# Performance work log

Hardware: AMD Instinct MI355X
Metric: run time of the kernel (lower is better)

Reference implementation:

```python
import jax, jax.numpy as jnp
import numpy as np


def setup_inputs() -> dict:
    key = jax.random.key(0)
    k1, k2, k3, k4 = jax.random.split(key, 4)
    B, n_env, in_ch, out_ch, code_ch, modes1, L = 16, 8, 32, 32, 16, 64, 8192
    scale = 1.0 / (in_ch * out_ch)
    return {
        "x": jax.random.normal(k1, (B, n_env * in_ch, L), dtype=jnp.float32),
        "codes": jax.random.normal(k2, (n_env, code_ch), dtype=jnp.float32),
        "com_weights": scale * jax.random.uniform(k3, (in_ch, out_ch, modes1, 2), dtype=jnp.float32),
        "code_weights": scale * jax.random.uniform(k4, (code_ch * in_ch, out_ch, modes1, 2), dtype=jnp.float32),
        "filter_weights": -3.0 * jnp.ones((modes1,), dtype=jnp.float32),
    }


def _as_complex(w):
    return w[..., 0] + 1j * w[..., 1]


def reference(x, codes, com_weights, code_weights, filter_weights):
    B, C, L = x.shape
    n_env, code_ch = codes.shape
    in_ch = C // n_env
    out_ch = com_weights.shape[1]
    modes1 = com_weights.shape[2]
    n_freq = L // 2 + 1

    # FFT and reshape to [B, e, i, freq]
    x_ft = jnp.fft.rfft(x).reshape(B, n_env, in_ch, n_freq)
    xm = x_ft[..., :modes1]  # mode truncation

    cw = _as_complex(com_weights)  # [i, o, m]
    codew = _as_complex(code_weights.reshape(code_ch, in_ch, out_ch, modes1, 2))  # [c,i,o,m]
    env_w = jnp.einsum('ec,ciom->eiom', codes.astype(codew.dtype), codew)

    # hardsigmoid(filter_weights): clip(x/6 + 0.5, 0, 1)
    lam = jnp.clip(filter_weights / 6.0 + 0.5, 0.0, 1.0)  # [m]

    out_m = (lam * jnp.einsum('beim,iom->beom', xm, cw)
             + (1.0 - lam) * jnp.einsum('beim,eiom->beom', xm, env_w))  # [B,e,o,m]

    # zero-pad back to full spectrum then inverse FFT
    out_ft = jnp.zeros((B, n_env, out_ch, n_freq), dtype=out_m.dtype)
    out_ft = out_ft.at[..., :modes1].set(out_m)
    out_ft = out_ft.reshape(B, n_env * out_ch, n_freq)
    return jnp.fft.irfft(out_ft, n=L)
```

## Files before the change

### kernel.cpp

```cpp
#include <hip/hip_runtime.h>
#include <hip/hip_bf16.h>
#include <math.h>
#include <stdint.h>

typedef __bf16 bf16_t;
typedef __bf16 bf16x8 __attribute__((ext_vector_type(8)));
typedef float  f32x4  __attribute__((ext_vector_type(4)));

#define L_LEN 8192
#define MODES 64
#define NCOMP 128
#define M_ROWS 4096

__device__ __forceinline__ void g2lds16(const void* g, void* l) {
  __builtin_amdgcn_global_load_lds(
      (__attribute__((address_space(1))) void*)(uintptr_t)(g),
      (__attribute__((address_space(3))) void*)(l), 16, 0, 0);
}

__global__ void gen_basis(bf16_t* __restrict__ B1t, bf16_t* __restrict__ B1) {
  int id = blockIdx.x * 256 + threadIdx.x;
  int l = id >> 6;
  int k = id & 63;
  int r = (l * k) & (L_LEN - 1);
  float ang = (float)r * 7.6699039394282061e-4f;
  float s, c;
  sincosf(ang, &s, &c);
  B1 [l * NCOMP + k]             = (bf16_t)c;
  B1 [l * NCOMP + MODES + k]     = (bf16_t)(-s);
  B1t[(size_t)k * L_LEN + l]           = (bf16_t)c;
  B1t[(size_t)(MODES + k) * L_LEN + l] = (bf16_t)(-s);
}

__global__ void wmix(const float* __restrict__ codes, const float* __restrict__ comw,
                     const float* __restrict__ codew, const float* __restrict__ fw,
                     float* __restrict__ W) {
  int id = blockIdx.x * 256 + threadIdx.x;
  int k = id & 63;
  int o = (id >> 6) & 31;
  int i = (id >> 11) & 31;
  int e = id >> 16;
  float lam = fminf(fmaxf(fw[k] * (1.0f / 6.0f) + 0.5f, 0.0f), 1.0f);
  float are = 0.f, aim = 0.f;
#pragma unroll
  for (int c = 0; c < 16; ++c) {
    float cd = codes[e * 16 + c];
    const float* p = codew + ((((c * 32 + i) * 32 + o) * 64 + k) << 1);
    are += cd * p[0];
    aim += cd * p[1];
  }
  const float* q = comw + (((i * 32 + o) * 64 + k) << 1);
  float wre = lam * q[0] + (1.f - lam) * are;
  float wim = lam * q[1] + (1.f - lam) * aim;
  float* dst = W + ((((e * 32 + i) * 32 + o) * 64 + k) << 1);
  dst[0] = wre;
  dst[1] = wim;
}

__global__ __launch_bounds__(256) void stage1(const float* __restrict__ x,
                                              const bf16_t* __restrict__ B1t,
                                              float* __restrict__ X) {
  __shared__ bf16_t Al[128 * 72];
  __shared__ bf16_t Bl[128 * 64];
  const int t = threadIdx.x;
  const int lane = t & 63;
  const int w = t >> 6;
  const int wm = w >> 1, wn = w & 1;
  const int mt = blockIdx.x;
  const int sp = blockIdx.y;
  const int lq = lane >> 4;
  const int l15 = lane & 15;

  f32x4 acc[4][4];
#pragma unroll
  for (int a = 0; a < 4; ++a)
#pragma unroll
    for (int b = 0; b < 4; ++b) acc[a][b] = (f32x4){0.f, 0.f, 0.f, 0.f};

  const int r = t >> 1, half = t & 1;
  const float* xrow = x + (size_t)(mt * 128 + r) * L_LEN + half * 32;
  bf16_t* adst = Al + r * 72 + half * 32;

  for (int ch = 0; ch < 8; ++ch) {
    const int l0 = sp * 512 + ch * 64;
    __syncthreads();
    const float4* xp = (const float4*)(xrow + l0);
#pragma unroll
    for (int j = 0; j < 4; ++j) {
      float4 p0 = xp[2 * j], p1 = xp[2 * j + 1];
      bf16x8 v = {(bf16_t)p0.x, (bf16_t)p0.y, (bf16_t)p0.z, (bf16_t)p0.w,
                  (bf16_t)p1.x, (bf16_t)p1.y, (bf16_t)p1.z, (bf16_t)p1.w};
      *(bf16x8*)(adst + j * 8) = v;
    }
#pragma unroll
    for (int q2 = 0; q2 < 4; ++q2) {
      int slot = t + 256 * q2;
      int n  = slot >> 3;
      int m8 = slot & 7;
      int j8 = m8 ^ (n & 7);
      g2lds16(B1t + (size_t)n * L_LEN + l0 + j8 * 8, (char*)Bl + slot * 16);
    }
    __syncthreads();
#pragma unroll
    for (int s = 0; s < 2; ++s) {
      bf16x8 a[4], b[4];
#pragma unroll
      for (int mf = 0; mf < 4; ++mf) {
        int row = wm * 64 + mf * 16 + l15;
        a[mf] = *(const bf16x8*)(Al + row * 72 + s * 32 + lq * 8);
      }
#pragma unroll
      for (int nf = 0; nf < 4; ++nf) {
        int n = wn * 64 + nf * 16 + l15;
        int j8 = (s * 4 + lq) ^ (n & 7);
        b[nf] = *(const bf16x8*)(Bl + n * 64 + j8 * 8);
      }
#pragma unroll
      for (int mf = 0; mf < 4; ++mf)
#pragma unroll
        for (int nf = 0; nf < 4; ++nf)
          acc[mf][nf] = __builtin_amdgcn_mfma_f32_16x16x32_bf16(a[mf], b[nf], acc[mf][nf], 0, 0, 0);
    }
  }
#pragma unroll
  for (int mf = 0; mf < 4; ++mf)
#pragma unroll
    for (int nf = 0; nf < 4; ++nf) {
      int n = wn * 64 + nf * 16 + l15;
#pragma unroll
      for (int rg = 0; rg < 4; ++rg) {
        int m = mt * 128 + wm * 64 + mf * 16 + lq * 4 + rg;
        atomicAdd(X + (size_t)m * NCOMP + n, acc[mf][nf][rg]);
      }
    }
}

__global__ __launch_bounds__(256) void mixk(const float* __restrict__ X,
                                            const float* __restrict__ W,
                                            bf16_t* __restrict__ A2) {
  __shared__ float Xs[32 * 128];
  const int t = threadIdx.x;
  const int be = blockIdx.x;
  const int e = be & 7;
#pragma unroll
  for (int j = 0; j < 16; ++j) {
    int idx = t + 256 * j;
    Xs[idx] = X[(size_t)be * 4096 + idx];
  }
  __syncthreads();
  const int k = t & 63;
  const int olo = t >> 6;
  float yre[8], yim[8];
#pragma unroll
  for (int j = 0; j < 8; ++j) { yre[j] = 0.f; yim[j] = 0.f; }
  for (int i = 0; i < 32; ++i) {
    float xr = Xs[i * 128 + k];
    float xi = Xs[i * 128 + 64 + k];
    const float* wp = W + ((((e * 32 + i) * 32 + olo * 8) * 64 + k) << 1);
#pragma unroll
    for (int j = 0; j < 8; ++j) {
      float2 wv = *(const float2*)(wp + j * 128);
      yre[j] += xr * wv.x - xi * wv.y;
      yim[j] += xr * wv.y + xi * wv.x;
    }
  }
  float sc = (k == 0) ? (1.0f / 8192.0f) : (2.0f / 8192.0f);
#pragma unroll
  for (int j = 0; j < 8; ++j) {
    int m = be * 32 + olo * 8 + j;
    A2[m * NCOMP + k]         = (bf16_t)(yre[j] * sc);
    A2[m * NCOMP + MODES + k] = (bf16_t)(yim[j] * sc);
  }
}

__global__ __launch_bounds__(256) void stage2(const bf16_t* __restrict__ A2,
                                              const bf16_t* __restrict__ B1,
                                              float* __restrict__ out) {
  __shared__ bf16_t As[128 * 128];
  __shared__ bf16_t Bs[128 * 128];
  const int t = threadIdx.x;
  const int lane = t & 63;
  const int w = t >> 6;
  const int wm = w >> 1, wl = w & 1;
  const int lt = blockIdx.x, mt = blockIdx.y;
  const int lq = lane >> 4, l15 = lane & 15;

#pragma unroll
  for (int q2 = 0; q2 < 8; ++q2) {
    int slot = t + 256 * q2;
    int row = slot >> 4;
    int m16 = slot & 15;
    int j8 = m16 ^ (row & 15);
    g2lds16(A2 + (size_t)(mt * 128 + row) * NCOMP + j8 * 8, (char*)As + slot * 16);
  }
#pragma unroll
  for (int q2 = 0; q2 < 8; ++q2) {
    int slot = t + 256 * q2;
    int lr = slot >> 4;
    int m16 = slot & 15;
    int j8 = m16 ^ (lr & 15);
    g2lds16(B1 + (size_t)(lt * 128 + lr) * NCOMP + j8 * 8, (char*)Bs + slot * 16);
  }
  __syncthreads();

  f32x4 acc[4][4];
#pragma unroll
  for (int a = 0; a < 4; ++a)
#pragma unroll
    for (int b = 0; b < 4; ++b) acc[a][b] = (f32x4){0.f, 0.f, 0.f, 0.f};

#pragma unroll
  for (int s = 0; s < 4; ++s) {
    bf16x8 a[4], b[4];
#pragma unroll
    for (int mf = 0; mf < 4; ++mf) {
      int row = wm * 64 + mf * 16 + l15;
      a[mf] = *(const bf16x8*)(As + row * 128 + (((s * 4 + lq) ^ (row & 15)) * 8));
    }
#pragma unroll
    for (int nf = 0; nf < 4; ++nf) {
      int lr = wl * 64 + nf * 16 + l15;
      b[nf] = *(const bf16x8*)(Bs + lr * 128 + (((s * 4 + lq) ^ (lr & 15)) * 8));
    }
#pragma unroll
    for (int mf = 0; mf < 4; ++mf)
#pragma unroll
      for (int nf = 0; nf < 4; ++nf)
        acc[mf][nf] = __builtin_amdgcn_mfma_f32_16x16x32_bf16(a[mf], b[nf], acc[mf][nf], 0, 0, 0);
  }

#pragma unroll
  for (int mf = 0; mf < 4; ++mf)
#pragma unroll
    for (int nf = 0; nf < 4; ++nf) {
      int m = mt * 128 + wm * 64 + mf * 16 + lq * 4;
      int l = lt * 128 + wl * 64 + nf * 16 + l15;
      float* op = out + (size_t)m * L_LEN + l;
#pragma unroll
      for (int rg = 0; rg < 4; ++rg) op[(size_t)rg * L_LEN] = acc[mf][nf][rg];
    }
}

extern "C" void kernel_launch(void* const* d_in, const int* in_sizes, int n_in,
                              void* d_out, int out_size, void* d_ws, size_t ws_size,
                              hipStream_t stream) {
  const float* x     = (const float*)d_in[0];
  const float* codes = (const float*)d_in[1];
  const float* comw  = (const float*)d_in[2];
  const float* codew = (const float*)d_in[3];
  const float* fw    = (const float*)d_in[4];
  float* out = (float*)d_out;
  char* ws = (char*)d_ws;
  bf16_t* B1t = (bf16_t*)(ws);
  bf16_t* B1  = (bf16_t*)(ws + (size_t)(2u << 20));
  float*  X   = (float*) (ws + (size_t)(4u << 20));
  float*  W   = (float*) (ws + (size_t)(6u << 20));
  bf16_t* A2  = (bf16_t*)(ws + (size_t)(10u << 20));

  gen_basis<<<2048, 256, 0, stream>>>(B1t, B1);
  wmix<<<2048, 256, 0, stream>>>(codes, comw, codew, fw, W);
  hipMemsetAsync(X, 0, (size_t)M_ROWS * NCOMP * sizeof(float), stream);
  stage1<<<dim3(32, 16), 256, 0, stream>>>(x, B1t, X);
  mixk<<<128, 256, 0, stream>>>(X, W, A2);
  stage2<<<dim3(64, 32), 256, 0, stream>>>(A2, B1, out);
}
```

Baseline: 306.4 us.

## Drop LDS staging in GEMMs, split basis generation, use hardware sin/cos

Both DFT GEMM stages now load MFMA fragments straight from global memory into registers instead of staging tiles through shared memory, which removes the barriers and LDS traffic. stage1 is retiled to 64-row blocks with half the accumulators, so twice as many blocks launch. Basis generation is split into two kernels: the transposed basis is written with coalesced vector stores, and both use the hardware sin/cos builtins on normalized turns instead of sincosf. Risks are redundant global and L2 reads with uncoalesced fragment loads, and lower precision from the hardware trig, though bf16 rounding likely hides that.

```diff
diff --git a/kernel.cpp b/kernel.cpp
--- a/kernel.cpp
+++ b/kernel.cpp
@@ -4,6 +4,7 @@
 #include <stdint.h>
 
 typedef __bf16 bf16_t;
+typedef __bf16 bf16x4v __attribute__((ext_vector_type(4)));
 typedef __bf16 bf16x8 __attribute__((ext_vector_type(8)));
 typedef float  f32x4  __attribute__((ext_vector_type(4)));
 
@@ -12,24 +13,30 @@
 #define NCOMP 128
 #define M_ROWS 4096
 
-__device__ __forceinline__ void g2lds16(const void* g, void* l) {
-  __builtin_amdgcn_global_load_lds(
-      (__attribute__((address_space(1))) void*)(uintptr_t)(g),
-      (__attribute__((address_space(3))) void*)(l), 16, 0, 0);
-}
-
-__global__ void gen_basis(bf16_t* __restrict__ B1t, bf16_t* __restrict__ B1) {
+__global__ void gen_b1(bf16_t* __restrict__ B1) {
   int id = blockIdx.x * 256 + threadIdx.x;
   int l = id >> 6;
   int k = id & 63;
-  int r = (l * k) & (L_LEN - 1);
-  float ang = (float)r * 7.6699039394282061e-4f;
-  float s, c;
-  sincosf(ang, &s, &c);
-  B1 [l * NCOMP + k]             = (bf16_t)c;
-  B1 [l * NCOMP + MODES + k]     = (bf16_t)(-s);
-  B1t[(size_t)k * L_LEN + l]           = (bf16_t)c;
-  B1t[(size_t)(MODES + k) * L_LEN + l] = (bf16_t)(-s);
+  float fr = (float)((l * k) & (L_LEN - 1)) * (1.0f / 8192.0f);
+  float c = __builtin_amdgcn_cosf(fr);
+  float s = __builtin_amdgcn_sinf(fr);
+  B1[l * NCOMP + k]         = (bf16_t)c;
+  B1[l * NCOMP + MODES + k] = (bf16_t)(-s);
+}
+
+__global__ void gen_b1t(bf16_t* __restrict__ B1t) {
+  int id = blockIdx.x * 256 + threadIdx.x;
+  int k  = id >> 11;
+  int l0 = (id & 2047) * 4;
+  bf16x4v cv, sv;
+#pragma unroll
+  for (int j = 0; j < 4; ++j) {
+    float fr = (float)(((l0 + j) * k) & (L_LEN - 1)) * (1.0f / 8192.0f);
+    cv[j] = (bf16_t)__builtin_amdgcn_cosf(fr);
+    sv[j] = (bf16_t)(-__builtin_amdgcn_sinf(fr));
+  }
+  *(bf16x4v*)(B1t + (size_t)k * L_LEN + l0)        = cv;
+  *(bf16x4v*)(B1t + (size_t)(k + 64) * L_LEN + l0) = sv;
 }
 
 __global__ void wmix(const float* __restrict__ codes, const float* __restrict__ comw,
@@ -60,76 +67,54 @@
 __global__ __launch_bounds__(256) void stage1(const float* __restrict__ x,
                                               const bf16_t* __restrict__ B1t,
                                               float* __restrict__ X) {
-  __shared__ bf16_t Al[128 * 72];
-  __shared__ bf16_t Bl[128 * 64];
   const int t = threadIdx.x;
   const int lane = t & 63;
   const int w = t >> 6;
   const int wm = w >> 1, wn = w & 1;
   const int mt = blockIdx.x;
   const int sp = blockIdx.y;
-  const int lq = lane >> 4;
-  const int l15 = lane & 15;
-
-  f32x4 acc[4][4];
-#pragma unroll
-  for (int a = 0; a < 4; ++a)
+  const int lq = lane >> 4, l15 = lane & 15;
+  const int mbase = mt * 64 + wm * 32;
+
+  f32x4 acc[2][4];
+#pragma unroll
+  for (int a = 0; a < 2; ++a)
 #pragma unroll
     for (int b = 0; b < 4; ++b) acc[a][b] = (f32x4){0.f, 0.f, 0.f, 0.f};
 
-  const int r = t >> 1, half = t & 1;
-  const float* xrow = x + (size_t)(mt * 128 + r) * L_LEN + half * 32;
-  bf16_t* adst = Al + r * 72 + half * 32;
-
-  for (int ch = 0; ch < 8; ++ch) {
-    const int l0 = sp * 512 + ch * 64;
-    __syncthreads();
-    const float4* xp = (const float4*)(xrow + l0);
-#pragma unroll
-    for (int j = 0; j < 4; ++j) {
-      float4 p0 = xp[2 * j], p1 = xp[2 * j + 1];
-      bf16x8 v = {(bf16_t)p0.x, (bf16_t)p0.y, (bf16_t)p0.z, (bf16_t)p0.w,
-                  (bf16_t)p1.x, (bf16_t)p1.y, (bf16_t)p1.z, (bf16_t)p1.w};
-      *(bf16x8*)(adst + j * 8) = v;
-    }
-#pragma unroll
-    for (int q2 = 0; q2 < 4; ++q2) {
-      int slot = t + 256 * q2;
-      int n  = slot >> 3;
-      int m8 = slot & 7;
-      int j8 = m8 ^ (n & 7);
-      g2lds16(B1t + (size_t)n * L_LEN + l0 + j8 * 8, (char*)Bl + slot * 16);
-    }
-    __syncthreads();
-#pragma unroll
-    for (int s = 0; s < 2; ++s) {
-      bf16x8 a[4], b[4];
-#pragma unroll
-      for (int mf = 0; mf < 4; ++mf) {
-        int row = wm * 64 + mf * 16 + l15;
-        a[mf] = *(const bf16x8*)(Al + row * 72 + s * 32 + lq * 8);
-      }
-#pragma unroll
-      for (int nf = 0; nf < 4; ++nf) {
-        int n = wn * 64 + nf * 16 + l15;
-        int j8 = (s * 4 + lq) ^ (n & 7);
-        b[nf] = *(const bf16x8*)(Bl + n * 64 + j8 * 8);
-      }
-#pragma unroll
-      for (int mf = 0; mf < 4; ++mf)
-#pragma unroll
-        for (int nf = 0; nf < 4; ++nf)
-          acc[mf][nf] = __builtin_amdgcn_mfma_f32_16x16x32_bf16(a[mf], b[nf], acc[mf][nf], 0, 0, 0);
-    }
-  }
-#pragma unroll
-  for (int mf = 0; mf < 4; ++mf)
+  const float*  xr0 = x + (size_t)(mbase + l15) * L_LEN + lq * 8;
+  const bf16_t* bp0 = B1t + (size_t)(wn * 64 + l15) * L_LEN + lq * 8;
+
+#pragma unroll 2
+  for (int ks = 0; ks < 16; ++ks) {
+    const int k0 = sp * 512 + ks * 32;
+    bf16x8 a[2];
+#pragma unroll
+    for (int mf = 0; mf < 2; ++mf) {
+      const float4* ap = (const float4*)(xr0 + (size_t)mf * 16 * L_LEN + k0);
+      float4 p0 = ap[0], p1 = ap[1];
+      a[mf] = (bf16x8){(bf16_t)p0.x, (bf16_t)p0.y, (bf16_t)p0.z, (bf16_t)p0.w,
+                       (bf16_t)p1.x, (bf16_t)p1.y, (bf16_t)p1.z, (bf16_t)p1.w};
+    }
+    bf16x8 b[4];
+#pragma unroll
+    for (int nf = 0; nf < 4; ++nf)
+      b[nf] = *(const bf16x8*)(bp0 + (size_t)nf * 16 * L_LEN + k0);
+#pragma unroll
+    for (int mf = 0; mf < 2; ++mf)
+#pragma unroll
+      for (int nf = 0; nf < 4; ++nf)
+        acc[mf][nf] = __builtin_amdgcn_mfma_f32_16x16x32_bf16(a[mf], b[nf], acc[mf][nf], 0, 0, 0);
+  }
+
+#pragma unroll
+  for (int mf = 0; mf < 2; ++mf)
 #pragma unroll
     for (int nf = 0; nf < 4; ++nf) {
       int n = wn * 64 + nf * 16 + l15;
 #pragma unroll
       for (int rg = 0; rg < 4; ++rg) {
-        int m = mt * 128 + wm * 64 + mf * 16 + lq * 4 + rg;
+        int m = mbase + mf * 16 + lq * 4 + rg;
         atomicAdd(X + (size_t)m * NCOMP + n, acc[mf][nf][rg]);
       }
     }
@@ -176,8 +161,6 @@
 __global__ __launch_bounds__(256) void stage2(const bf16_t* __restrict__ A2,
                                               const bf16_t* __restrict__ B1,
                                               float* __restrict__ out) {
-  __shared__ bf16_t As[128 * 128];
-  __shared__ bf16_t Bs[128 * 128];
   const int t = threadIdx.x;
   const int lane = t & 63;
   const int w = t >> 6;
@@ -185,43 +168,24 @@
   const int lt = blockIdx.x, mt = blockIdx.y;
   const int lq = lane >> 4, l15 = lane & 15;
 
-#pragma unroll
-  for (int q2 = 0; q2 < 8; ++q2) {
-    int slot = t + 256 * q2;
-    int row = slot >> 4;
-    int m16 = slot & 15;
-    int j8 = m16 ^ (row & 15);
-    g2lds16(A2 + (size_t)(mt * 128 + row) * NCOMP + j8 * 8, (char*)As + slot * 16);
-  }
-#pragma unroll
-  for (int q2 = 0; q2 < 8; ++q2) {
-    int slot = t + 256 * q2;
-    int lr = slot >> 4;
-    int m16 = slot & 15;
-    int j8 = m16 ^ (lr & 15);
-    g2lds16(B1 + (size_t)(lt * 128 + lr) * NCOMP + j8 * 8, (char*)Bs + slot * 16);
-  }
-  __syncthreads();
-
   f32x4 acc[4][4];
 #pragma unroll
   for (int a = 0; a < 4; ++a)
 #pragma unroll
     for (int b = 0; b < 4; ++b) acc[a][b] = (f32x4){0.f, 0.f, 0.f, 0.f};
 
-#pragma unroll
+  const bf16_t* ap0 = A2 + (size_t)(mt * 128 + wm * 64 + l15) * NCOMP + lq * 8;
+  const bf16_t* bp0 = B1 + (size_t)(lt * 128 + wl * 64 + l15) * NCOMP + lq * 8;
+
+#pragma unroll 2
   for (int s = 0; s < 4; ++s) {
     bf16x8 a[4], b[4];
 #pragma unroll
-    for (int mf = 0; mf < 4; ++mf) {
-      int row = wm * 64 + mf * 16 + l15;
-      a[mf] = *(const bf16x8*)(As + row * 128 + (((s * 4 + lq) ^ (row & 15)) * 8));
-    }
-#pragma unroll
-    for (int nf = 0; nf < 4; ++nf) {
-      int lr = wl * 64 + nf * 16 + l15;
-      b[nf] = *(const bf16x8*)(Bs + lr * 128 + (((s * 4 + lq) ^ (lr & 15)) * 8));
-    }
+    for (int mf = 0; mf < 4; ++mf)
+      a[mf] = *(const bf16x8*)(ap0 + mf * 16 * NCOMP + s * 32);
+#pragma unroll
+    for (int nf = 0; nf < 4; ++nf)
+      b[nf] = *(const bf16x8*)(bp0 + nf * 16 * NCOMP + s * 32);
 #pragma unroll
     for (int mf = 0; mf < 4; ++mf)
 #pragma unroll
@@ -257,10 +221,11 @@
   float*  W   = (float*) (ws + (size_t)(6u << 20));
   bf16_t* A2  = (bf16_t*)(ws + (size_t)(10u << 20));
 
-  gen_basis<<<2048, 256, 0, stream>>>(B1t, B1);
+  gen_b1 <<<2048, 256, 0, stream>>>(B1);
+  gen_b1t<<<512, 256, 0, stream>>>(B1t);
   wmix<<<2048, 256, 0, stream>>>(codes, comw, codew, fw, W);
   hipMemsetAsync(X, 0, (size_t)M_ROWS * NCOMP * sizeof(float), stream);
-  stage1<<<dim3(32, 16), 256, 0, stream>>>(x, B1t, X);
+  stage1<<<dim3(64, 16), 256, 0, stream>>>(x, B1t, X);
   mixk<<<128, 256, 0, stream>>>(X, W, A2);
   stage2<<<dim3(64, 32), 256, 0, stream>>>(A2, B1, out);
 }
```

New measurement: 336.4 us. +9.8%, slower.
